# Kernel tuning notes

Measured on AMD Instinct MI355X. Metric: run time of the kernel, lower is better.

## Reference

```python
import jax, jax.numpy as jnp
import numpy as np

N = 4096
E = 131072
IN_C, HID, HEADS, OUT_C = 512, 64, 8, 256
BETA = 0.5
NEG_SLOPE = 0.2


def _glorot(key, shape, fan_in, fan_out):
    lim = float(np.sqrt(6.0 / (fan_in + fan_out)))
    return jax.random.uniform(key, shape, jnp.float32, -lim, lim)


def setup_inputs() -> dict:
    key = jax.random.key(0)
    ks = jax.random.split(key, 12)
    x = jax.random.normal(ks[0], (N, IN_C), jnp.float32)
    src = jax.random.randint(ks[1], (E,), 0, N)
    dst = jax.random.randint(ks[2], (E,), 0, N)
    dst = jnp.where(src == dst, (dst + 1) % N, dst)  # no self loops (module removes then re-adds)
    edge_index = jnp.stack([src, dst]).astype(jnp.int64)
    # layer 1: in=512 -> heads=8, out=64 (concat -> 512), residual=False
    W1 = _glorot(ks[3], (IN_C, HEADS * HID), IN_C, HEADS * HID)
    as1 = _glorot(ks[4], (HEADS, HID), HID, HID)
    ad1 = _glorot(ks[5], (HEADS, HID), HID, HID)
    b1 = jnp.zeros((HEADS * HID,), jnp.float32)
    # layer 2: in=512 -> heads=1, out=256, concat=False, residual=True (res_linear needed)
    W2 = _glorot(ks[6], (HEADS * HID, OUT_C), HEADS * HID, OUT_C)
    as2 = _glorot(ks[7], (1, OUT_C), OUT_C, OUT_C)
    ad2 = _glorot(ks[8], (1, OUT_C), OUT_C, OUT_C)
    b2 = jnp.zeros((OUT_C,), jnp.float32)
    resW2 = _glorot(ks[9], (HEADS * HID, OUT_C), HEADS * HID, OUT_C)
    return {"x": x, "edge_index": edge_index, "W1": W1, "as1": as1, "ad1": ad1,
            "b1": b1, "W2": W2, "as2": as2, "ad2": ad2, "b2": b2, "resW2": resW2}


def _seg_softmax(e, seg, n):
    # numerically-stable softmax over edges grouped by destination node
    m = jax.ops.segment_max(e, seg, num_segments=n)  # [n, H]
    a = jnp.exp(e - m[seg])
    s = jax.ops.segment_sum(a, seg, num_segments=n)
    return a / (s[seg] + 1e-16)


def _motif_gat_layer(x, edge_index, W, a_src, a_dst, bias, res_W, heads, out_ch, concat):
    n = x.shape[0]
    residual = x
    h = (x @ W).reshape(n, heads, out_ch)
    # add self loops (input edge_index has none)
    loops = jnp.arange(n, dtype=edge_index.dtype)
    src = jnp.concatenate([edge_index[0], loops])
    dst = jnp.concatenate([edge_index[1], loops])
    xj = h[src]  # [E', H, C]
    xi = h[dst]
    e = (xj * a_src[None]).sum(-1) + (xi * a_dst[None]).sum(-1)  # [E', H]
    alpha_first = _seg_softmax(jax.nn.leaky_relu(e, NEG_SLOPE), dst, n)
    # motif adjacency: dense A^3, row-normalized by clamped row sum
    adj = jnp.zeros((n, n), x.dtype).at[src, dst].set(1.0)
    m3 = adj @ adj @ adj
    m3 = m3 / jnp.clip(m3.sum(-1, keepdims=True), 1.0)
    mw = m3[src, dst][:, None]  # [E', 1]
    alpha_motif = _seg_softmax(jax.nn.leaky_relu(e * mw, NEG_SLOPE), dst, n)
    alpha = BETA * alpha_first + (1.0 - BETA) * alpha_motif  # dropout: eval mode -> identity
    out = jax.ops.segment_sum(alpha[:, :, None] * xj, dst, num_segments=n)  # [n, H, C]
    out = out.reshape(n, heads * out_ch) if concat else out.mean(1)
    if res_W is not None:
        out = out + residual @ res_W
    return out + bias


def reference(x, edge_index, W1, as1, ad1, b1, W2, as2, ad2, b2, resW2):
    h = _motif_gat_layer(x, edge_index, W1, as1, ad1, b1, None, HEADS, HID, True)
    h = jax.nn.elu(h)  # dropout: eval mode -> identity
    out = _motif_gat_layer(h, edge_index, W2, as2, ad2, b2, resW2, 1, OUT_C, False)
    return out
```

## Files before the change

### kernel.cpp

```cpp
#include <hip/hip_runtime.h>
#include <hip/hip_bf16.h>
#include <math.h>

#define NN 4096
#define EE 131072
#define EP (EE + NN)
#define C1 512
#define H1 8
#define C2 256
#define NWORDS 128
#define KP 520

typedef __attribute__((ext_vector_type(8))) short bf16x8;
typedef __attribute__((ext_vector_type(4))) float f32x4;

__device__ __forceinline__ float wredMaxf(float v){
#pragma unroll
  for(int o=32;o;o>>=1) v = fmaxf(v, __shfl_xor(v,o));
  return v;
}
__device__ __forceinline__ float wredSumf(float v){
#pragma unroll
  for(int o=32;o;o>>=1) v += __shfl_xor(v,o);
  return v;
}
__device__ __forceinline__ int wredSumi(int v){
#pragma unroll
  for(int o=32;o;o>>=1) v += __shfl_xor(v,o);
  return v;
}

__device__ __forceinline__ void bfsplit(float v, unsigned short& h, unsigned short& l){
  unsigned bits = __float_as_uint(v);
  h = (unsigned short)(bits>>16);
  float hf = __uint_as_float(bits & 0xFFFF0000u);
  float lo = v - hf;
  l = (unsigned short)(__float_as_uint(lo)>>16);
}

__device__ __forceinline__ int detect_mode(const int* __restrict__ ei32){
  unsigned nz = 0;
#pragma unroll
  for(int i=1;i<16;i+=2) nz |= (unsigned)ei32[i];
  return nz != 0;
}

__device__ __forceinline__ void edge_sd(const int* ei32, int mode, int e, int& s, int& d){
  if(e < EE){
    if(mode==0){ s = ei32[2*e]; d = ei32[2*(EE+e)]; }
    else       { s = ei32[e];   d = ei32[EE+e]; }
  } else { s = e - EE; d = s; }
}

__global__ __launch_bounds__(256) void k_build(const int* __restrict__ ei32,
    unsigned* __restrict__ rowbits, unsigned* __restrict__ colbits, unsigned* __restrict__ cnt){
  int e = blockIdx.x*256 + threadIdx.x;
  if(e >= EP) return;
  int m = detect_mode(ei32), s, d;
  edge_sd(ei32, m, e, s, d);
  atomicOr(&rowbits[s*NWORDS + (d>>5)], 1u<<(d&31));
  atomicOr(&colbits[d*NWORDS + (s>>5)], 1u<<(s&31));
  atomicAdd(&cnt[d], 1u);
}

__global__ __launch_bounds__(256) void k_scan(const unsigned* __restrict__ cnt, unsigned* __restrict__ rowptr){
  __shared__ unsigned part[256];
  int t = threadIdx.x;
  unsigned loc[16]; unsigned s = 0;
#pragma unroll
  for(int i=0;i<16;i++){ loc[i]=cnt[t*16+i]; s+=loc[i]; }
  part[t]=s; __syncthreads();
  for(int off=1;off<256;off<<=1){
    unsigned v = (t>=off)? part[t-off] : 0u;
    __syncthreads();
    part[t]+=v;
    __syncthreads();
  }
  unsigned run = (t==0)? 0u : part[t-1];
#pragma unroll
  for(int i=0;i<16;i++){ rowptr[t*16+i]=run; run+=loc[i]; }
  if(t==255) rowptr[NN]=run;
}

__global__ __launch_bounds__(256) void k_fill(const int* __restrict__ ei32,
    const unsigned* __restrict__ rowptr, unsigned* __restrict__ fill,
    unsigned* __restrict__ csr_src){
  int e = blockIdx.x*256 + threadIdx.x;
  if(e >= EP) return;
  int m = detect_mode(ei32), s, d;
  edge_sd(ei32, m, e, s, d);
  unsigned pos = rowptr[d] + atomicAdd(&fill[d], 1u);
  csr_src[pos]=(unsigned)s;
}

__global__ __launch_bounds__(256) void k_deg(const unsigned* __restrict__ rowbits, float* __restrict__ v1){
  int node = blockIdx.x*4 + (threadIdx.x>>6);
  int lane = threadIdx.x & 63;
  unsigned w0 = rowbits[node*NWORDS + 2*lane];
  unsigned w1 = rowbits[node*NWORDS + 2*lane + 1];
  int c = __popc(w0) + __popc(w1);
  c = wredSumi(c);
  if(lane==0) v1[node] = (float)c;
}

__global__ __launch_bounds__(256) void k_mv(const unsigned* __restrict__ rowbits,
    const float* __restrict__ vin, float* __restrict__ vout){
  int node = blockIdx.x*4 + (threadIdx.x>>6);
  int lane = threadIdx.x & 63;
  float sum = 0.f;
  unsigned w = rowbits[node*NWORDS + 2*lane]; int b0 = lane*64;
  while(w){ int b=__ffs(w)-1; sum += vin[b0+b]; w &= w-1; }
  w = rowbits[node*NWORDS + 2*lane + 1]; b0 = lane*64 + 32;
  while(w){ int b=__ffs(w)-1; sum += vin[b0+b]; w &= w-1; }
  sum = wredSumf(sum);
  if(lane==0) vout[node] = sum;
}

__global__ __launch_bounds__(64) void k_motif(const unsigned* __restrict__ rowbits, const unsigned* __restrict__ colbits,
    const unsigned* __restrict__ rowptr, const unsigned* __restrict__ csr_src,
    const float* __restrict__ v3, float* __restrict__ mwc){
  int d = blockIdx.x;
  int lane = threadIdx.x;
  __shared__ unsigned short nbr[1024];
  __shared__ int cntL;
  if(lane==0) cntL=0;
  __syncthreads();
  {
    unsigned w = colbits[d*NWORDS + 2*lane]; int b0 = lane*64;
    while(w){ int b=__ffs(w)-1; int pos=atomicAdd(&cntL,1); nbr[pos]=(unsigned short)(b0+b); w&=w-1; }
    w = colbits[d*NWORDS + 2*lane + 1]; b0 = lane*64 + 32;
    while(w){ int b=__ffs(w)-1; int pos=atomicAdd(&cntL,1); nbr[pos]=(unsigned short)(b0+b); w&=w-1; }
  }
  __syncthreads();
  int m = cntL;
  unsigned gp[8][2];
#pragma unroll
  for(int p=0;p<8;p++){ gp[p][0]=0u; gp[p][1]=0u; }
  for(int t0=0;t0<m;t0+=4){
    unsigned xa[4], xb[4];
#pragma unroll
    for(int j=0;j<4;j++){
      int tt=t0+j;
      if(tt<m){ int l = nbr[tt]; xa[j]=colbits[l*NWORDS+2*lane]; xb[j]=colbits[l*NWORDS+2*lane+1]; }
      else    { xa[j]=0u; xb[j]=0u; }
    }
#pragma unroll
    for(int j=0;j<4;j++){
      unsigned c = xa[j];
#pragma unroll
      for(int p=0;p<8;p++){ unsigned cy = gp[p][0] & c; gp[p][0] ^= c; c = cy; }
      c = xb[j];
#pragma unroll
      for(int p=0;p<8;p++){ unsigned cy = gp[p][1] & c; gp[p][1] ^= c; c = cy; }
    }
  }
  unsigned base = rowptr[d], deg = rowptr[d+1]-base;
  for(unsigned i0=0;i0<deg;i0+=4){
    unsigned sidx[4], ra[4], rb[4];
#pragma unroll
    for(int j=0;j<4;j++){
      unsigned ii = (i0+j < deg) ? (i0+j) : (deg-1);
      sidx[j] = csr_src[base+ii];
    }
#pragma unroll
    for(int j=0;j<4;j++){ ra[j]=rowbits[sidx[j]*NWORDS+2*lane]; rb[j]=rowbits[sidx[j]*NWORDS+2*lane+1]; }
    int sum[4];
#pragma unroll
    for(int j=0;j<4;j++){
      int s=0;
#pragma unroll
      for(int p=0;p<8;p++)
        s += (__popc(ra[j]&gp[p][0]) + __popc(rb[j]&gp[p][1])) << p;
      sum[j]=s;
    }
    int pk0 = sum[0] | (sum[1]<<16);
    int pk1 = sum[2] | (sum[3]<<16);
    pk0 = wredSumi(pk0); pk1 = wredSumi(pk1);
    if(lane==0){
      int ss[4] = { pk0 & 0xFFFF, (pk0>>16)&0xFFFF, pk1 & 0xFFFF, (pk1>>16)&0xFFFF };
#pragma unroll
      for(int j=0;j<4;j++){
        unsigned idx = i0+j;
        if(idx<deg)
          mwc[base+idx] = (float)ss[j] / fmaxf(v3[csr_src[base+idx]], 1.0f);
      }
    }
  }
}

__global__ __launch_bounds__(256) void k_cvtA(const float* __restrict__ X,
    unsigned short* __restrict__ xh, unsigned short* __restrict__ xl){
  int e = blockIdx.x*256 + threadIdx.x;
  int row = e >> 6;
  int c0 = (e & 63) * 8;
  const float4 v0 = *(const float4*)&X[(size_t)row*C1 + c0];
  const float4 v1 = *(const float4*)&X[(size_t)row*C1 + c0 + 4];
  float vv[8] = {v0.x,v0.y,v0.z,v0.w,v1.x,v1.y,v1.z,v1.w};
  unsigned short h[8], l[8];
#pragma unroll
  for(int j=0;j<8;j++) bfsplit(vv[j], h[j], l[j]);
  *(bf16x8*)&xh[(size_t)row*KP + c0] = *(bf16x8*)h;
  *(bf16x8*)&xl[(size_t)row*KP + c0] = *(bf16x8*)l;
}

__global__ __launch_bounds__(256) void k_cvtB_all(const float* __restrict__ W1f,
    const float* __restrict__ W2f, const float* __restrict__ Wrf,
    unsigned short* __restrict__ b1h, unsigned short* __restrict__ b1l,
    unsigned short* __restrict__ b2h, unsigned short* __restrict__ b2l){
  int blk = blockIdx.x; int t = threadIdx.x;
  const float* W; int N, n, nrow; unsigned short *bh, *bl;
  if(blk < 512){ W=W1f; N=512; n=blk;     nrow=n;     bh=b1h; bl=b1l; }
  else if(blk < 768){ W=W2f; N=256; n=blk-512; nrow=n;     bh=b2h; bl=b2l; }
  else { W=Wrf; N=256; n=blk-768; nrow=n+256; bh=b2h; bl=b2l; }
  int k = t*2;
  float a = W[(size_t)k*N + n];
  float b = W[(size_t)(k+1)*N + n];
  unsigned short h0,l0,h1,l1;
  bfsplit(a,h0,l0); bfsplit(b,h1,l1);
  unsigned short hp[2]={h0,h1}, lp[2]={l0,l1};
  *(unsigned int*)&bh[(size_t)nrow*KP + k] = *(unsigned int*)hp;
  *(unsigned int*)&bl[(size_t)nrow*KP + k] = *(unsigned int*)lp;
}

__global__ __launch_bounds__(256) void k_gemm_mfma(
    const unsigned short* __restrict__ Ah, const unsigned short* __restrict__ Al,
    const unsigned short* __restrict__ Bh, const unsigned short* __restrict__ Bl,
    float* __restrict__ C, int M, int N){
  __shared__ unsigned short Ahs[64][72], Als[64][72], Bhs[64][72], Bls[64][72];
  int bm = blockIdx.y*64, bn = blockIdx.x*64;
  int t = threadIdx.x, lane = t&63, w = t>>6;
  int wm = (w>>1)*32, wn = (w&1)*32;
  f32x4 acc[2][2];
#pragma unroll
  for(int i=0;i<2;i++)
#pragma unroll
    for(int j=0;j<2;j++) acc[i][j] = (f32x4){0.f,0.f,0.f,0.f};
  int sm = t>>2, sk = (t&3)*16;
  const unsigned short* pAh = &Ah[(size_t)(bm+sm)*KP + sk];
  const unsigned short* pAl = &Al[(size_t)(bm+sm)*KP + sk];
  const unsigned short* pBh = &Bh[(size_t)(bn+sm)*KP + sk];
  const unsigned short* pBl = &Bl[(size_t)(bn+sm)*KP + sk];
  int fr = lane&15, kg = lane>>4;
  bf16x8 rah0 = *(const bf16x8*)(pAh), rah1 = *(const bf16x8*)(pAh+8);
  bf16x8 ral0 = *(const bf16x8*)(pAl), ral1 = *(const bf16x8*)(pAl+8);
  bf16x8 rbh0 = *(const bf16x8*)(pBh), rbh1 = *(const bf16x8*)(pBh+8);
  bf16x8 rbl0 = *(const bf16x8*)(pBl), rbl1 = *(const bf16x8*)(pBl+8);
  *(bf16x8*)&Ahs[sm][sk] = rah0; *(bf16x8*)&Ahs[sm][sk+8] = rah1;
  *(bf16x8*)&Als[sm][sk] = ral0; *(bf16x8*)&Als[sm][sk+8] = ral1;
  *(bf16x8*)&Bhs[sm][sk] = rbh0; *(bf16x8*)&Bhs[sm][sk+8] = rbh1;
  *(bf16x8*)&Bls[sm][sk] = rbl0; *(bf16x8*)&Bls[sm][sk+8] = rbl1;
  __syncthreads();
  for(int k0=0;k0<C1;k0+=64){
    int kn = k0+64;
    if(kn<C1){
      rah0 = *(const bf16x8*)(pAh+kn); rah1 = *(const bf16x8*)(pAh+kn+8);
      ral0 = *(const bf16x8*)(pAl+kn); ral1 = *(const bf16x8*)(pAl+kn+8);
      rbh0 = *(const bf16x8*)(pBh+kn); rbh1 = *(const bf16x8*)(pBh+kn+8);
      rbl0 = *(const bf16x8*)(pBl+kn); rbl1 = *(const bf16x8*)(pBl+kn+8);
    }
#pragma unroll
    for(int ks=0;ks<64;ks+=32){
      bf16x8 fah[2], fal[2], fbh[2], fbl[2];
#pragma unroll
      for(int i=0;i<2;i++){
        fah[i] = *(bf16x8*)&Ahs[wm + i*16 + fr][ks + kg*8];
        fal[i] = *(bf16x8*)&Als[wm + i*16 + fr][ks + kg*8];
        fbh[i] = *(bf16x8*)&Bhs[wn + i*16 + fr][ks + kg*8];
        fbl[i] = *(bf16x8*)&Bls[wn + i*16 + fr][ks + kg*8];
      }
#pragma unroll
      for(int i=0;i<2;i++)
#pragma unroll
        for(int j=0;j<2;j++){
          acc[i][j] = __builtin_amdgcn_mfma_f32_16x16x32_bf16(fah[i], fbh[j], acc[i][j], 0,0,0);
          acc[i][j] = __builtin_amdgcn_mfma_f32_16x16x32_bf16(fah[i], fbl[j], acc[i][j], 0,0,0);
          acc[i][j] = __builtin_amdgcn_mfma_f32_16x16x32_bf16(fal[i], fbh[j], acc[i][j], 0,0,0);
        }
    }
    __syncthreads();
    if(kn<C1){
      *(bf16x8*)&Ahs[sm][sk] = rah0; *(bf16x8*)&Ahs[sm][sk+8] = rah1;
      *(bf16x8*)&Als[sm][sk] = ral0; *(bf16x8*)&Als[sm][sk+8] = ral1;
      *(bf16x8*)&Bhs[sm][sk] = rbh0; *(bf16x8*)&Bhs[sm][sk+8] = rbh1;
      *(bf16x8*)&Bls[sm][sk] = rbl0; *(bf16x8*)&Bls[sm][sk+8] = rbl1;
    }
    __syncthreads();
  }
#pragma unroll
  for(int i=0;i<2;i++)
#pragma unroll
    for(int j=0;j<2;j++){
      int gr = bm + wm + i*16 + kg*4;
      int gc = bn + wn + j*16 + fr;
#pragma unroll
      for(int e=0;e<4;e++)
        C[(size_t)(gr+e)*N + gc] = acc[i][j][e];
    }
}

__global__ __launch_bounds__(512) void k_attn1(const float* __restrict__ hpre, const float* __restrict__ as1,
    const float* __restrict__ ad1, float* __restrict__ asrc, float* __restrict__ adst){
  int n = blockIdx.x; int t = threadIdx.x; int lane = t&63; int h = t>>6;
  float v = hpre[n*C1 + t];
  float p1 = v*as1[t], p2 = v*ad1[t];
  p1 = wredSumf(p1); p2 = wredSumf(p2);
  if(lane==0){ asrc[n*H1+h]=p1; adst[n*H1+h]=p2; }
}

__global__ __launch_bounds__(128) void k_layer1(const unsigned* __restrict__ rowptr, const unsigned* __restrict__ csr_src,
    const float* __restrict__ mwc, const float* __restrict__ asrc, const float* __restrict__ adst,
    const float* __restrict__ hpre, const float* __restrict__ b1,
    unsigned short* __restrict__ h1h, unsigned short* __restrict__ h1l){
  int n = blockIdx.x;
  int tid = threadIdx.x, lane = tid&63, wv = tid>>6;
  unsigned base = rowptr[n], deg = rowptr[n+1]-base;
  __shared__ float a1s[128][9];
  __shared__ float a2s[128][9];
  __shared__ unsigned ssrc[128];
  __shared__ float red1[2][8], red2[2][8];
  __shared__ float snm1[8], snm2[8], sscl1[8], sscl2[8];
  __shared__ float sS1[8], sS2[8], sM1[8], sM2[8];
  __shared__ float adsts[8];
  if(tid<8){ adsts[tid]=adst[n*H1+tid]; sM1[tid]=-3.0e38f; sM2[tid]=-3.0e38f; sS1[tid]=0.f; sS2[tid]=0.f; }
  __syncthreads();
  int h = tid>>4;
  float4 acc1={0.f,0.f,0.f,0.f}, acc2={0.f,0.f,0.f,0.f};
  for(unsigned c0=0;c0<deg;c0+=128){
    int csz = (int)min(128u, deg-c0);
    bool act = (tid < csz);
    float el[8], em[8];
    if(act){
      unsigned s = csr_src[base+c0+tid];
      ssrc[tid]=s;
      float mwv = mwc[base+c0+tid];
      const float4 a0v = *(const float4*)&asrc[s*H1];
      const float4 a1v = *(const float4*)&asrc[s*H1+4];
      float as8[8]={a0v.x,a0v.y,a0v.z,a0v.w,a1v.x,a1v.y,a1v.z,a1v.w};
#pragma unroll
      for(int hh=0;hh<8;hh++){
        float ev = as8[hh]+adsts[hh];
        el[hh] = ev>=0.f? ev : 0.2f*ev;
        float evm = ev*mwv;
        em[hh] = evm>=0.f? evm : 0.2f*evm;
      }
    } else {
#pragma unroll
      for(int hh=0;hh<8;hh++){ el[hh]=-3.0e38f; em[hh]=-3.0e38f; }
    }
    float mx1[8], mx2[8];
#pragma unroll
    for(int hh=0;hh<8;hh++){ mx1[hh]=wredMaxf(el[hh]); mx2[hh]=wredMaxf(em[hh]); }
    if(lane==0){
#pragma unroll
      for(int hh=0;hh<8;hh++){ red1[wv][hh]=mx1[hh]; red2[wv][hh]=mx2[hh]; }
    }
    __syncthreads();
    if(tid<8){
      float cm1 = fmaxf(red1[0][tid], red1[1][tid]);
      float cm2 = fmaxf(red2[0][tid], red2[1][tid]);
      float nm1 = fmaxf(sM1[tid], cm1), nm2 = fmaxf(sM2[tid], cm2);
      sscl1[tid] = expf(sM1[tid]-nm1); sscl2[tid] = expf(sM2[tid]-nm2);
      snm1[tid]=nm1; snm2[tid]=nm2;
      sM1[tid]=nm1;  sM2[tid]=nm2;
    }
    __syncthreads();
    float s1l[8], s2l[8];
#pragma unroll
    for(int hh=0;hh<8;hh++){
      float a1v = act? expf(el[hh]-snm1[hh]) : 0.f;
      float a2v = act? expf(em[hh]-snm2[hh]) : 0.f;
      if(act){ a1s[tid][hh]=a1v; a2s[tid][hh]=a2v; }
      s1l[hh]=a1v; s2l[hh]=a2v;
    }
#pragma unroll
    for(int hh=0;hh<8;hh++){ s1l[hh]=wredSumf(s1l[hh]); s2l[hh]=wredSumf(s2l[hh]); }
    if(lane==0){
#pragma unroll
      for(int hh=0;hh<8;hh++){ red1[wv][hh]=s1l[hh]; red2[wv][hh]=s2l[hh]; }
    }
    __syncthreads();
    if(tid<8){
      sS1[tid] = sS1[tid]*sscl1[tid] + red1[0][tid]+red1[1][tid];
      sS2[tid] = sS2[tid]*sscl2[tid] + red2[0][tid]+red2[1][tid];
    }
    {
      float sc1 = sscl1[h], sc2 = sscl2[h];
      acc1.x*=sc1; acc1.y*=sc1; acc1.z*=sc1; acc1.w*=sc1;
      acc2.x*=sc2; acc2.y*=sc2; acc2.z*=sc2; acc2.w*=sc2;
    }
    for(int i0=0;i0<csz;i0+=8){
      int jn = min(8, csz-i0);
      unsigned sj[8]; float a1j[8], a2j[8];
#pragma unroll
      for(int j=0;j<8;j++){
        int ii = (j<jn)? i0+j : i0;
        sj[j]=ssrc[ii]; a1j[j]=a1s[ii][h]; a2j[j]=a2s[ii][h];
      }
      float4 hv[8];
#pragma unroll
      for(int j=0;j<8;j++) hv[j] = *(const float4*)&hpre[(size_t)sj[j]*C1 + tid*4];
#pragma unroll
      for(int j=0;j<8;j++){
        float w1 = (j<jn)? a1j[j] : 0.f;
        float w2 = (j<jn)? a2j[j] : 0.f;
        acc1.x += w1*hv[j].x; acc1.y += w1*hv[j].y; acc1.z += w1*hv[j].z; acc1.w += w1*hv[j].w;
        acc2.x += w2*hv[j].x; acc2.y += w2*hv[j].y; acc2.z += w2*hv[j].z; acc2.w += w2*hv[j].w;
      }
    }
    __syncthreads();
  }
  float r1 = 0.5f/(sS1[h]+1e-16f), r2 = 0.5f/(sS2[h]+1e-16f);
  int cc = tid*4;
  const float4 bv = *(const float4*)&b1[cc];
  float o[4];
  float vx = acc1.x*r1 + acc2.x*r2 + bv.x; o[0] = vx>0.f? vx : expm1f(vx);
  float vy = acc1.y*r1 + acc2.y*r2 + bv.y; o[1] = vy>0.f? vy : expm1f(vy);
  float vz = acc1.z*r1 + acc2.z*r2 + bv.z; o[2] = vz>0.f? vz : expm1f(vz);
  float vw = acc1.w*r1 + acc2.w*r2 + bv.w; o[3] = vw>0.f? vw : expm1f(vw);
  unsigned short hh4[4], ll4[4];
#pragma unroll
  for(int j=0;j<4;j++) bfsplit(o[j], hh4[j], ll4[j]);
  *(ushort4*)&h1h[(size_t)n*KP + cc] = *(ushort4*)hh4;
  *(ushort4*)&h1l[(size_t)n*KP + cc] = *(ushort4*)ll4;
}

__global__ __launch_bounds__(64) void k_attn2(const float* __restrict__ h2, const float* __restrict__ as2,
    const float* __restrict__ ad2, float* __restrict__ asrc, float* __restrict__ adst){
  int n = blockIdx.x; int lane = threadIdx.x;
  const float4 hv = *(const float4*)&h2[(size_t)n*512 + lane*4];
  const float4 av = *(const float4*)&as2[lane*4];
  const float4 dv = *(const float4*)&ad2[lane*4];
  float p1 = hv.x*av.x + hv.y*av.y + hv.z*av.z + hv.w*av.w;
  float p2 = hv.x*dv.x + hv.y*dv.y + hv.z*dv.z + hv.w*dv.w;
  p1 = wredSumf(p1); p2 = wredSumf(p2);
  if(lane==0){ asrc[n]=p1; adst[n]=p2; }
}

__global__ __launch_bounds__(64) void k_layer2(const unsigned* __restrict__ rowptr, const unsigned* __restrict__ csr_src,
    const float* __restrict__ mwc, const float* __restrict__ asrc, const float* __restrict__ adst,
    const float* __restrict__ h2, const float* __restrict__ res,
    const float* __restrict__ b2, float* __restrict__ out){
  int n = blockIdx.x; int lane = threadIdx.x;
  unsigned base = rowptr[n], deg = rowptr[n+1]-base;
  __shared__ float a1s[64], a2s[64];
  __shared__ unsigned ssrc[64];
  float ad = adst[n];
  float M1=-3.0e38f, M2=-3.0e38f, S1=0.f, S2=0.f;
  float4 acc1={0.f,0.f,0.f,0.f}, acc2={0.f,0.f,0.f,0.f};
  for(unsigned c0=0;c0<deg;c0+=64){
    int csz = (int)min(64u, deg-c0);
    bool act = (lane < csz);
    float el=-3.0e38f, em=-3.0e38f;
    if(act){
      unsigned s = csr_src[base+c0+lane];
      ssrc[lane]=s;
      float mwv = mwc[base+c0+lane];
      float ev = asrc[s] + ad;
      el = ev>=0.f? ev : 0.2f*ev;
      float evm = ev*mwv;
      em = evm>=0.f? evm : 0.2f*evm;
    }
    float nm1 = fmaxf(M1, wredMaxf(el));
    float nm2 = fmaxf(M2, wredMaxf(em));
    float sc1 = expf(M1-nm1), sc2 = expf(M2-nm2);
    M1=nm1; M2=nm2;
    float a1 = act? expf(el-nm1) : 0.f;
    float a2 = act? expf(em-nm2) : 0.f;
    if(act){ a1s[lane]=a1; a2s[lane]=a2; }
    S1 = S1*sc1 + wredSumf(a1);
    S2 = S2*sc2 + wredSumf(a2);
    acc1.x*=sc1; acc1.y*=sc1; acc1.z*=sc1; acc1.w*=sc1;
    acc2.x*=sc2; acc2.y*=sc2; acc2.z*=sc2; acc2.w*=sc2;
    __syncthreads();
    for(int i0=0;i0<csz;i0+=8){
      int jn = min(8, csz-i0);
      unsigned sj[8]; float a1j[8], a2j[8];
#pragma unroll
      for(int j=0;j<8;j++){
        int ii = (j<jn)? i0+j : i0;
        sj[j]=ssrc[ii]; a1j[j]=a1s[ii]; a2j[j]=a2s[ii];
      }
      float4 hv[8];
#pragma unroll
      for(int j=0;j<8;j++) hv[j] = *(const float4*)&h2[(size_t)sj[j]*512 + lane*4];
#pragma unroll
      for(int j=0;j<8;j++){
        float w1 = (j<jn)? a1j[j] : 0.f;
        float w2 = (j<jn)? a2j[j] : 0.f;
        acc1.x += w1*hv[j].x; acc1.y += w1*hv[j].y; acc1.z += w1*hv[j].z; acc1.w += w1*hv[j].w;
        acc2.x += w2*hv[j].x; acc2.y += w2*hv[j].y; acc2.z += w2*hv[j].z; acc2.w += w2*hv[j].w;
      }
    }
    __syncthreads();
  }
  float r1 = 0.5f/(S1+1e-16f), r2 = 0.5f/(S2+1e-16f);
  int cc = lane*4;
  const float4 rv = *(const float4*)&res[(size_t)n*512 + cc];
  const float4 bv = *(const float4*)&b2[cc];
  float4 o = {acc1.x*r1 + acc2.x*r2 + rv.x + bv.x,
              acc1.y*r1 + acc2.y*r2 + rv.y + bv.y,
              acc1.z*r1 + acc2.z*r2 + rv.z + bv.z,
              acc1.w*r1 + acc2.w*r2 + rv.w + bv.w};
  *(float4*)&out[(size_t)n*C2 + cc] = o;
}

extern "C" void kernel_launch(void* const* d_in, const int* in_sizes, int n_in,
                              void* d_out, int out_size, void* d_ws, size_t ws_size,
                              hipStream_t stream) {
  const float* x    = (const float*)d_in[0];
  const int*   ei32 = (const int*)d_in[1];
  const float* W1   = (const float*)d_in[2];
  const float* as1  = (const float*)d_in[3];
  const float* ad1  = (const float*)d_in[4];
  const float* b1   = (const float*)d_in[5];
  const float* W2   = (const float*)d_in[6];
  const float* as2  = (const float*)d_in[7];
  const float* ad2  = (const float*)d_in[8];
  const float* b2   = (const float*)d_in[9];
  const float* resW2= (const float*)d_in[10];
  float* out = (float*)d_out;

  char* p = (char*)d_ws;
  auto alloc = [&](size_t b){ void* r=(void*)p; p += (b + 255) & ~(size_t)255; return r; };
  unsigned* rowbits = (unsigned*)alloc((size_t)NN*NWORDS*4);
  unsigned* colbits = (unsigned*)alloc((size_t)NN*NWORDS*4);
  unsigned* cnt     = (unsigned*)alloc(NN*4);
  unsigned* fill    = (unsigned*)alloc(NN*4);
  size_t zbytes = (size_t)NN*NWORDS*4*2 + (size_t)NN*4*2;
  unsigned* rowptr  = (unsigned*)alloc((NN+4)*4);
  float* v1 = (float*)alloc(NN*4);
  float* v2 = (float*)alloc(NN*4);
  float* v3 = (float*)alloc(NN*4);
  unsigned* csr_src = (unsigned*)alloc((size_t)EP*4);
  float* mwc  = (float*)alloc((size_t)EP*4);
  float* asrc1= (float*)alloc(NN*H1*4);
  float* adst1= (float*)alloc(NN*H1*4);
  unsigned short* xsh = (unsigned short*)alloc((size_t)NN*KP*2);
  unsigned short* xsl = (unsigned short*)alloc((size_t)NN*KP*2);
  unsigned short* bt1h= (unsigned short*)alloc((size_t)C1*KP*2);
  unsigned short* bt1l= (unsigned short*)alloc((size_t)C1*KP*2);
  unsigned short* bt2h= (unsigned short*)alloc((size_t)C1*KP*2);
  unsigned short* bt2l= (unsigned short*)alloc((size_t)C1*KP*2);
  float* hpre = (float*)alloc((size_t)NN*C1*4);
  unsigned short* h1h = (unsigned short*)alloc((size_t)NN*KP*2);
  unsigned short* h1l = (unsigned short*)alloc((size_t)NN*KP*2);
  float* c23  = (float*)alloc((size_t)NN*512*4);
  float* asrc2= (float*)alloc(NN*4);
  float* adst2= (float*)alloc(NN*4);
  float* h2  = c23;
  float* res = c23 + 256;

  hipMemsetAsync(rowbits, 0, zbytes, stream);

  k_build<<<(EP+255)/256,256,0,stream>>>(ei32, rowbits, colbits, cnt);
  k_scan<<<1,256,0,stream>>>(cnt, rowptr);
  k_fill<<<(EP+255)/256,256,0,stream>>>(ei32, rowptr, fill, csr_src);
  k_deg<<<NN/4,256,0,stream>>>(rowbits, v1);
  k_mv<<<NN/4,256,0,stream>>>(rowbits, v1, v2);
  k_mv<<<NN/4,256,0,stream>>>(rowbits, v2, v3);
  k_motif<<<NN,64,0,stream>>>(rowbits, colbits, rowptr, csr_src, v3, mwc);

  k_cvtA<<<(NN*64)/256,256,0,stream>>>(x, xsh, xsl);
  k_cvtB_all<<<1024,256,0,stream>>>(W1, W2, resW2, bt1h, bt1l, bt2h, bt2l);

  k_gemm_mfma<<<dim3(C1/64, NN/64),256,0,stream>>>(xsh, xsl, bt1h, bt1l, hpre, NN, C1);
  k_attn1<<<NN,512,0,stream>>>(hpre, as1, ad1, asrc1, adst1);
  k_layer1<<<NN,128,0,stream>>>(rowptr, csr_src, mwc, asrc1, adst1, hpre, b1, h1h, h1l);

  k_gemm_mfma<<<dim3(512/64, NN/64),256,0,stream>>>(h1h, h1l, bt2h, bt2l, c23, NN, 512);
  k_attn2<<<NN,64,0,stream>>>(h2, as2, ad2, asrc2, adst2);
  k_layer2<<<NN,64,0,stream>>>(rowptr, csr_src, mwc, asrc2, adst2, h2, res, b2, out);
}
```

Measured before the change: 253.6 us.

## Merge independent preprocessing kernels and fuse attention projections into GEMM epilogue

```diff
diff --git a/kernel.cpp b/kernel.cpp
--- a/kernel.cpp
+++ b/kernel.cpp
@@ -63,57 +63,105 @@
   atomicAdd(&cnt[d], 1u);
 }
 
-__global__ __launch_bounds__(256) void k_scan(const unsigned* __restrict__ cnt, unsigned* __restrict__ rowptr){
-  __shared__ unsigned part[256];
+__global__ __launch_bounds__(256) void k_scan_deg(const unsigned* __restrict__ cnt, unsigned* __restrict__ rowptr,
+    const unsigned* __restrict__ rowbits, float* __restrict__ v1){
   int t = threadIdx.x;
-  unsigned loc[16]; unsigned s = 0;
-#pragma unroll
-  for(int i=0;i<16;i++){ loc[i]=cnt[t*16+i]; s+=loc[i]; }
-  part[t]=s; __syncthreads();
-  for(int off=1;off<256;off<<=1){
-    unsigned v = (t>=off)? part[t-off] : 0u;
-    __syncthreads();
-    part[t]+=v;
-    __syncthreads();
-  }
-  unsigned run = (t==0)? 0u : part[t-1];
-#pragma unroll
-  for(int i=0;i<16;i++){ rowptr[t*16+i]=run; run+=loc[i]; }
-  if(t==255) rowptr[NN]=run;
-}
-
-__global__ __launch_bounds__(256) void k_fill(const int* __restrict__ ei32,
-    const unsigned* __restrict__ rowptr, unsigned* __restrict__ fill,
-    unsigned* __restrict__ csr_src){
-  int e = blockIdx.x*256 + threadIdx.x;
-  if(e >= EP) return;
-  int m = detect_mode(ei32), s, d;
-  edge_sd(ei32, m, e, s, d);
-  unsigned pos = rowptr[d] + atomicAdd(&fill[d], 1u);
-  csr_src[pos]=(unsigned)s;
-}
-
-__global__ __launch_bounds__(256) void k_deg(const unsigned* __restrict__ rowbits, float* __restrict__ v1){
-  int node = blockIdx.x*4 + (threadIdx.x>>6);
-  int lane = threadIdx.x & 63;
-  unsigned w0 = rowbits[node*NWORDS + 2*lane];
-  unsigned w1 = rowbits[node*NWORDS + 2*lane + 1];
-  int c = __popc(w0) + __popc(w1);
-  c = wredSumi(c);
-  if(lane==0) v1[node] = (float)c;
-}
-
-__global__ __launch_bounds__(256) void k_mv(const unsigned* __restrict__ rowbits,
-    const float* __restrict__ vin, float* __restrict__ vout){
-  int node = blockIdx.x*4 + (threadIdx.x>>6);
-  int lane = threadIdx.x & 63;
-  float sum = 0.f;
-  unsigned w = rowbits[node*NWORDS + 2*lane]; int b0 = lane*64;
-  while(w){ int b=__ffs(w)-1; sum += vin[b0+b]; w &= w-1; }
-  w = rowbits[node*NWORDS + 2*lane + 1]; b0 = lane*64 + 32;
-  while(w){ int b=__ffs(w)-1; sum += vin[b0+b]; w &= w-1; }
-  sum = wredSumf(sum);
-  if(lane==0) vout[node] = sum;
+  if(blockIdx.x == 0){
+    __shared__ unsigned part[256];
+    unsigned loc[16]; unsigned s = 0;
+#pragma unroll
+    for(int i=0;i<16;i++){ loc[i]=cnt[t*16+i]; s+=loc[i]; }
+    part[t]=s; __syncthreads();
+    for(int off=1;off<256;off<<=1){
+      unsigned v = (t>=off)? part[t-off] : 0u;
+      __syncthreads();
+      part[t]+=v;
+      __syncthreads();
+    }
+    unsigned run = (t==0)? 0u : part[t-1];
+#pragma unroll
+    for(int i=0;i<16;i++){ rowptr[t*16+i]=run; run+=loc[i]; }
+    if(t==255) rowptr[NN]=run;
+  } else {
+    int node = (blockIdx.x-1)*4 + (t>>6);
+    int lane = t & 63;
+    unsigned w0 = rowbits[node*NWORDS + 2*lane];
+    unsigned w1 = rowbits[node*NWORDS + 2*lane + 1];
+    int c = __popc(w0) + __popc(w1);
+    c = wredSumi(c);
+    if(lane==0) v1[node] = (float)c;
+  }
+}
+
+__global__ __launch_bounds__(256) void k_fill_mv(const int* __restrict__ ei32,
+    const unsigned* __restrict__ rowptr, unsigned* __restrict__ fill, unsigned* __restrict__ csr_src,
+    const unsigned* __restrict__ rowbits, const float* __restrict__ v1, float* __restrict__ v2){
+  int t = threadIdx.x;
+  if(blockIdx.x < 528){
+    int e = blockIdx.x*256 + t;
+    if(e >= EP) return;
+    int m = detect_mode(ei32), s, d;
+    edge_sd(ei32, m, e, s, d);
+    unsigned pos = rowptr[d] + atomicAdd(&fill[d], 1u);
+    csr_src[pos]=(unsigned)s;
+  } else {
+    int node = (blockIdx.x-528)*4 + (t>>6);
+    int lane = t & 63;
+    float sum = 0.f;
+    unsigned w = rowbits[node*NWORDS + 2*lane]; int b0 = lane*64;
+    while(w){ int b=__ffs(w)-1; sum += v1[b0+b]; w &= w-1; }
+    w = rowbits[node*NWORDS + 2*lane + 1]; b0 = lane*64 + 32;
+    while(w){ int b=__ffs(w)-1; sum += v1[b0+b]; w &= w-1; }
+    sum = wredSumf(sum);
+    if(lane==0) v2[node] = sum;
+  }
+}
+
+__global__ __launch_bounds__(256) void k_mv2_cvt(const unsigned* __restrict__ rowbits,
+    const float* __restrict__ v2, float* __restrict__ v3,
+    const float* __restrict__ X, unsigned short* __restrict__ xh, unsigned short* __restrict__ xl,
+    const float* __restrict__ W1f, const float* __restrict__ W2f, const float* __restrict__ Wrf,
+    unsigned short* __restrict__ b1h, unsigned short* __restrict__ b1l,
+    unsigned short* __restrict__ b2h, unsigned short* __restrict__ b2l){
+  int t = threadIdx.x;
+  int b = blockIdx.x;
+  if(b < 1024){
+    int node = b*4 + (t>>6);
+    int lane = t & 63;
+    float sum = 0.f;
+    unsigned w = rowbits[node*NWORDS + 2*lane]; int b0 = lane*64;
+    while(w){ int bb=__ffs(w)-1; sum += v2[b0+bb]; w &= w-1; }
+    w = rowbits[node*NWORDS + 2*lane + 1]; b0 = lane*64 + 32;
+    while(w){ int bb=__ffs(w)-1; sum += v2[b0+bb]; w &= w-1; }
+    sum = wredSumf(sum);
+    if(lane==0) v3[node] = sum;
+  } else if(b < 2048){
+    int e = (b-1024)*256 + t;
+    int row = e >> 6;
+    int c0 = (e & 63) * 8;
+    const float4 v0 = *(const float4*)&X[(size_t)row*C1 + c0];
+    const float4 v1q = *(const float4*)&X[(size_t)row*C1 + c0 + 4];
+    float vv[8] = {v0.x,v0.y,v0.z,v0.w,v1q.x,v1q.y,v1q.z,v1q.w};
+    unsigned short h[8], l[8];
+#pragma unroll
+    for(int j=0;j<8;j++) bfsplit(vv[j], h[j], l[j]);
+    *(bf16x8*)&xh[(size_t)row*KP + c0] = *(bf16x8*)h;
+    *(bf16x8*)&xl[(size_t)row*KP + c0] = *(bf16x8*)l;
+  } else {
+    int blk = b - 2048;
+    const float* W; int N, n, nrow; unsigned short *bh, *bl;
+    if(blk < 512){ W=W1f; N=512; n=blk;     nrow=n;     bh=b1h; bl=b1l; }
+    else if(blk < 768){ W=W2f; N=256; n=blk-512; nrow=n;     bh=b2h; bl=b2l; }
+    else { W=Wrf; N=256; n=blk-768; nrow=n+256; bh=b2h; bl=b2l; }
+    int k = t*2;
+    float a = W[(size_t)k*N + n];
+    float bb = W[(size_t)(k+1)*N + n];
+    unsigned short h0,l0,h1,l1;
+    bfsplit(a,h0,l0); bfsplit(bb,h1,l1);
+    unsigned short hp[2]={h0,h1}, lp[2]={l0,l1};
+    *(unsigned int*)&bh[(size_t)nrow*KP + k] = *(unsigned int*)hp;
+    *(unsigned int*)&bl[(size_t)nrow*KP + k] = *(unsigned int*)lp;
+  }
 }
 
 __global__ __launch_bounds__(64) void k_motif(const unsigned* __restrict__ rowbits, const unsigned* __restrict__ colbits,
@@ -188,44 +236,12 @@
   }
 }
 
-__global__ __launch_bounds__(256) void k_cvtA(const float* __restrict__ X,
-    unsigned short* __restrict__ xh, unsigned short* __restrict__ xl){
-  int e = blockIdx.x*256 + threadIdx.x;
-  int row = e >> 6;
-  int c0 = (e & 63) * 8;
-  const float4 v0 = *(const float4*)&X[(size_t)row*C1 + c0];
-  const float4 v1 = *(const float4*)&X[(size_t)row*C1 + c0 + 4];
-  float vv[8] = {v0.x,v0.y,v0.z,v0.w,v1.x,v1.y,v1.z,v1.w};
-  unsigned short h[8], l[8];
-#pragma unroll
-  for(int j=0;j<8;j++) bfsplit(vv[j], h[j], l[j]);
-  *(bf16x8*)&xh[(size_t)row*KP + c0] = *(bf16x8*)h;
-  *(bf16x8*)&xl[(size_t)row*KP + c0] = *(bf16x8*)l;
-}
-
-__global__ __launch_bounds__(256) void k_cvtB_all(const float* __restrict__ W1f,
-    const float* __restrict__ W2f, const float* __restrict__ Wrf,
-    unsigned short* __restrict__ b1h, unsigned short* __restrict__ b1l,
-    unsigned short* __restrict__ b2h, unsigned short* __restrict__ b2l){
-  int blk = blockIdx.x; int t = threadIdx.x;
-  const float* W; int N, n, nrow; unsigned short *bh, *bl;
-  if(blk < 512){ W=W1f; N=512; n=blk;     nrow=n;     bh=b1h; bl=b1l; }
-  else if(blk < 768){ W=W2f; N=256; n=blk-512; nrow=n;     bh=b2h; bl=b2l; }
-  else { W=Wrf; N=256; n=blk-768; nrow=n+256; bh=b2h; bl=b2l; }
-  int k = t*2;
-  float a = W[(size_t)k*N + n];
-  float b = W[(size_t)(k+1)*N + n];
-  unsigned short h0,l0,h1,l1;
-  bfsplit(a,h0,l0); bfsplit(b,h1,l1);
-  unsigned short hp[2]={h0,h1}, lp[2]={l0,l1};
-  *(unsigned int*)&bh[(size_t)nrow*KP + k] = *(unsigned int*)hp;
-  *(unsigned int*)&bl[(size_t)nrow*KP + k] = *(unsigned int*)lp;
-}
-
 __global__ __launch_bounds__(256) void k_gemm_mfma(
     const unsigned short* __restrict__ Ah, const unsigned short* __restrict__ Al,
     const unsigned short* __restrict__ Bh, const unsigned short* __restrict__ Bl,
-    float* __restrict__ C, int M, int N){
+    float* __restrict__ C, int M, int N,
+    const float* __restrict__ aS, const float* __restrict__ aD,
+    float* __restrict__ oS, float* __restrict__ oD, int amode){
   __shared__ unsigned short Ahs[64][72], Als[64][72], Bhs[64][72], Bls[64][72];
   int bm = blockIdx.y*64, bn = blockIdx.x*64;
   int t = threadIdx.x, lane = t&63, w = t>>6;
@@ -296,15 +312,42 @@
       for(int e=0;e<4;e++)
         C[(size_t)(gr+e)*N + gc] = acc[i][j][e];
     }
-}
-
-__global__ __launch_bounds__(512) void k_attn1(const float* __restrict__ hpre, const float* __restrict__ as1,
-    const float* __restrict__ ad1, float* __restrict__ asrc, float* __restrict__ adst){
-  int n = blockIdx.x; int t = threadIdx.x; int lane = t&63; int h = t>>6;
-  float v = hpre[n*C1 + t];
-  float p1 = v*as1[t], p2 = v*ad1[t];
-  p1 = wredSumf(p1); p2 = wredSumf(p2);
-  if(lane==0){ asrc[n*H1+h]=p1; adst[n*H1+h]=p2; }
+  bool do_attn = (amode==1) || (bn < 256);
+  if(do_attn){
+    float p1[2][4], p2[2][4];
+#pragma unroll
+    for(int i=0;i<2;i++)
+#pragma unroll
+      for(int e=0;e<4;e++){ p1[i][e]=0.f; p2[i][e]=0.f; }
+#pragma unroll
+    for(int j=0;j<2;j++){
+      int col = bn + wn + j*16 + fr;
+      float a1c = aS[col], a2c = aD[col];
+#pragma unroll
+      for(int i=0;i<2;i++)
+#pragma unroll
+        for(int e=0;e<4;e++){ p1[i][e] += acc[i][j][e]*a1c; p2[i][e] += acc[i][j][e]*a2c; }
+    }
+#pragma unroll
+    for(int o=1;o<16;o<<=1){
+#pragma unroll
+      for(int i=0;i<2;i++)
+#pragma unroll
+        for(int e=0;e<4;e++){ p1[i][e]+=__shfl_xor(p1[i][e],o); p2[i][e]+=__shfl_xor(p2[i][e],o); }
+    }
+    if(fr==0){
+      int head = (amode==1)? (bn>>6) : 0;
+      int hs = (amode==1)? H1 : 1;
+#pragma unroll
+      for(int i=0;i<2;i++)
+#pragma unroll
+        for(int e=0;e<4;e++){
+          int row = bm + wm + i*16 + kg*4 + e;
+          atomicAdd(&oS[row*hs + head], p1[i][e]);
+          atomicAdd(&oD[row*hs + head], p2[i][e]);
+        }
+    }
+  }
 }
 
 __global__ __launch_bounds__(128) void k_layer1(const unsigned* __restrict__ rowptr, const unsigned* __restrict__ csr_src,
@@ -424,18 +467,6 @@
   *(ushort4*)&h1l[(size_t)n*KP + cc] = *(ushort4*)ll4;
 }
 
-__global__ __launch_bounds__(64) void k_attn2(const float* __restrict__ h2, const float* __restrict__ as2,
-    const float* __restrict__ ad2, float* __restrict__ asrc, float* __restrict__ adst){
-  int n = blockIdx.x; int lane = threadIdx.x;
-  const float4 hv = *(const float4*)&h2[(size_t)n*512 + lane*4];
-  const float4 av = *(const float4*)&as2[lane*4];
-  const float4 dv = *(const float4*)&ad2[lane*4];
-  float p1 = hv.x*av.x + hv.y*av.y + hv.z*av.z + hv.w*av.w;
-  float p2 = hv.x*dv.x + hv.y*dv.y + hv.z*dv.z + hv.w*dv.w;
-  p1 = wredSumf(p1); p2 = wredSumf(p2);
-  if(lane==0){ asrc[n]=p1; adst[n]=p2; }
-}
-
 __global__ __launch_bounds__(64) void k_layer2(const unsigned* __restrict__ rowptr, const unsigned* __restrict__ csr_src,
     const float* __restrict__ mwc, const float* __restrict__ asrc, const float* __restrict__ adst,
     const float* __restrict__ h2, const float* __restrict__ res,
@@ -526,15 +557,17 @@
   unsigned* colbits = (unsigned*)alloc((size_t)NN*NWORDS*4);
   unsigned* cnt     = (unsigned*)alloc(NN*4);
   unsigned* fill    = (unsigned*)alloc(NN*4);
-  size_t zbytes = (size_t)NN*NWORDS*4*2 + (size_t)NN*4*2;
+  float* asrc1= (float*)alloc(NN*H1*4);
+  float* adst1= (float*)alloc(NN*H1*4);
+  float* asrc2= (float*)alloc(NN*4);
+  float* adst2= (float*)alloc(NN*4);
+  size_t zbytes = (size_t)(p - (char*)rowbits);
   unsigned* rowptr  = (unsigned*)alloc((NN+4)*4);
   float* v1 = (float*)alloc(NN*4);
   float* v2 = (float*)alloc(NN*4);
   float* v3 = (float*)alloc(NN*4);
   unsigned* csr_src = (unsigned*)alloc((size_t)EP*4);
   float* mwc  = (float*)alloc((size_t)EP*4);
-  float* asrc1= (float*)alloc(NN*H1*4);
-  float* adst1= (float*)alloc(NN*H1*4);
   unsigned short* xsh = (unsigned short*)alloc((size_t)NN*KP*2);
   unsigned short* xsl = (unsigned short*)alloc((size_t)NN*KP*2);
   unsigned short* bt1h= (unsigned short*)alloc((size_t)C1*KP*2);
@@ -545,29 +578,22 @@
   unsigned short* h1h = (unsigned short*)alloc((size_t)NN*KP*2);
   unsigned short* h1l = (unsigned short*)alloc((size_t)NN*KP*2);
   float* c23  = (float*)alloc((size_t)NN*512*4);
-  float* asrc2= (float*)alloc(NN*4);
-  float* adst2= (float*)alloc(NN*4);
   float* h2  = c23;
   float* res = c23 + 256;
 
   hipMemsetAsync(rowbits, 0, zbytes, stream);
 
   k_build<<<(EP+255)/256,256,0,stream>>>(ei32, rowbits, colbits, cnt);
-  k_scan<<<1,256,0,stream>>>(cnt, rowptr);
-  k_fill<<<(EP+255)/256,256,0,stream>>>(ei32, rowptr, fill, csr_src);
-  k_deg<<<NN/4,256,0,stream>>>(rowbits, v1);
-  k_mv<<<NN/4,256,0,stream>>>(rowbits, v1, v2);
-  k_mv<<<NN/4,256,0,stream>>>(rowbits, v2, v3);
+  k_scan_deg<<<1+NN/4,256,0,stream>>>(cnt, rowptr, rowbits, v1);
+  k_fill_mv<<<528+NN/4,256,0,stream>>>(ei32, rowptr, fill, csr_src, rowbits, v1, v2);
+  k_mv2_cvt<<<3072,256,0,stream>>>(rowbits, v2, v3, x, xsh, xsl, W1, W2, resW2, bt1h, bt1l, bt2h, bt2l);
   k_motif<<<NN,64,0,stream>>>(rowbits, colbits, rowptr, csr_src, v3, mwc);
 
-  k_cvtA<<<(NN*64)/256,256,0,stream>>>(x, xsh, xsl);
-  k_cvtB_all<<<1024,256,0,stream>>>(W1, W2, resW2, bt1h, bt1l, bt2h, bt2l);
-
-  k_gemm_mfma<<<dim3(C1/64, NN/64),256,0,stream>>>(xsh, xsl, bt1h, bt1l, hpre, NN, C1);
-  k_attn1<<<NN,512,0,stream>>>(hpre, as1, ad1, asrc1, adst1);
+  k_gemm_mfma<<<dim3(C1/64, NN/64),256,0,stream>>>(xsh, xsl, bt1h, bt1l, hpre, NN, C1,
+                                                   as1, ad1, asrc1, adst1, 1);
   k_layer1<<<NN,128,0,stream>>>(rowptr, csr_src, mwc, asrc1, adst1, hpre, b1, h1h, h1l);
 
-  k_gemm_mfma<<<dim3(512/64, NN/64),256,0,stream>>>(h1h, h1l, bt2h, bt2l, c23, NN, 512);
-  k_attn2<<<NN,64,0,stream>>>(h2, as2, ad2, asrc2, adst2);
+  k_gemm_mfma<<<dim3(512/64, NN/64),256,0,stream>>>(h1h, h1l, bt2h, bt2l, c23, NN, 512,
+                                                    as2, ad2, asrc2, adst2, 2);
   k_layer2<<<NN,64,0,stream>>>(rowptr, csr_src, mwc, asrc2, adst2, h2, res, b2, out);
 }
```

New measurement: 250.9 us. No clear change (-1.1%).
